# Kernel optimization log

Hardware: AMD Instinct MI355X
Metric: run time of the kernel (lower is better)

The kernel has to match this reference:

```python
import jax, jax.numpy as jnp
import numpy as np

SCORE_THRESHOLD = 0.05
IOU_THRESHOLD = 0.5
MAX_DETECTIONS = 300
NEG = -1e9  # sentinel for suppressed / below-threshold scores


def setup_inputs() -> dict:
    key = jax.random.key(0)
    k1, k2, k3, k4 = jax.random.split(key, 4)
    B, N, C = 8, 49104, 20
    # valid corner-format boxes [x1, y1, x2, y2] inside a 512x512 image
    ctr = jax.random.uniform(k1, (B, N, 2), minval=0.0, maxval=512.0)
    wh = jax.random.uniform(k2, (B, N, 2), minval=8.0, maxval=128.0)
    boxes = jnp.concatenate([ctr - wh / 2, ctr + wh / 2], axis=-1)
    boxes3D = jax.random.normal(k3, (B, N, 16), dtype=jnp.float32)
    classification = jax.random.uniform(k4, (B, N, C)) ** 2
    return {"boxes": boxes, "boxes3D": boxes3D, "classification": classification}


def _iou_one_vs_all(box, boxes, areas):
    # box [4], boxes [N,4], areas [N] -> iou [N]
    lt = jnp.maximum(box[:2], boxes[:, :2])
    rb = jnp.minimum(box[2:], boxes[:, 2:])
    wh = jnp.maximum(rb - lt, 0.0)
    inter = wh[:, 0] * wh[:, 1]
    area = (box[2] - box[0]) * (box[3] - box[1])
    return inter / (areas + area - inter + 1e-9)


def _nms_class(boxes, areas, scores):
    # greedy NMS for one class; fixed MAX_DETECTIONS iterations (jit-friendly)
    s0 = jnp.where(scores > SCORE_THRESHOLD, scores, NEG)
    n = scores.shape[0]
    arange_n = jnp.arange(n)

    def step(s, _):
        i = jnp.argmax(s)
        valid = s[i] > NEG / 2
        iou = _iou_one_vs_all(boxes[i], boxes, areas)
        sup = (iou > IOU_THRESHOLD) | (arange_n == i)
        s_new = jnp.where(valid & sup, NEG, s)
        return s_new, (i, jnp.where(valid, s[i], NEG))

    _, (idx, sel) = jax.lax.scan(step, s0, None, length=MAX_DETECTIONS)
    return idx, sel  # [MAX_DETECTIONS] each


def _filter_image(boxes, boxes3D, cls):
    # boxes [N,4], boxes3D [N,16], cls [N,C]
    areas = (boxes[:, 2] - boxes[:, 0]) * (boxes[:, 3] - boxes[:, 1])
    # per-class NMS, vectorized over classes
    idxs, scs = jax.vmap(lambda s: _nms_class(boxes, areas, s), in_axes=1)(cls)  # [C, MAX]
    C = cls.shape[1]
    labels = jnp.broadcast_to(jnp.arange(C)[:, None], idxs.shape)
    # global top-k across all class candidates (invalid ones carry NEG score)
    top_sc, top_i = jax.lax.top_k(scs.reshape(-1), MAX_DETECTIONS)
    sel_anchor = idxs.reshape(-1)[top_i]
    sel_lab = labels.reshape(-1)[top_i]
    ok = top_sc > NEG / 2
    out_boxes = jnp.where(ok[:, None], boxes[sel_anchor], -1.0)
    out_b3d = jnp.where(ok[:, None], boxes3D[sel_anchor], -1.0)
    out_sc = jnp.where(ok, top_sc, -1.0)
    out_lab = jnp.where(ok, sel_lab, -1).astype(jnp.int32)
    return out_boxes, out_b3d, out_sc, out_lab


def reference(boxes, boxes3D, classification):
    # map over batch, like backend.map_fn in the original
    return jax.vmap(_filter_image)(boxes, boxes3D, classification)
```

## Files before the change

### kernel.cpp

```cpp
#include <hip/hip_runtime.h>

#define NCLS    20
#define NB      8
#define MAXDET  300
#define NEGV    (-1e9f)
#define NEGH    (-5e8f)
#define BLKN    512
#define BLKC    1024
#define KTARGET 896
#define KMAX    1024
#define NBIN    256
#define NSLICE  64
#define SLSH    6
#define NSEG    8
#define SEGCAP  128
#define CSTR    16
#define T0F     0.98257f

#define T_MID   0x1.000001p-1

typedef unsigned long long u64;
typedef unsigned int u32;

__device__ __forceinline__ u64 packkey(float s, int j) {
    return ((u64)(__float_as_uint(s) ^ 0x80000000u) << 32) | (u32)(~(u32)j);
}
__device__ __forceinline__ u64 wredmax64(u64 k) {
#pragma unroll
    for (int off = 32; off > 0; off >>= 1) {
        u64 o = __shfl_xor(k, off);
        if (o > k) k = o;
    }
    return k;
}
__device__ __forceinline__ int binfull(float s) {
    int full = (int)(s * 262144.0f);
    return full > 262143 ? 262143 : full;
}
__device__ __forceinline__ int bin256(float s) { return binfull(s) >> 10; }

__global__ __launch_bounds__(256) void zero_kernel(u32* __restrict__ p, int nwords)
{
    int i = blockIdx.x * 256 + threadIdx.x;
    if (i < nwords) p[i] = 0;
}

__global__ __launch_bounds__(BLKN) void collect_kernel(
    const float* __restrict__ cls, u64* __restrict__ keys_g, u32* __restrict__ cnt_g, int n)
{
    const int b = blockIdx.x & 7;
    const int slice = blockIdx.x >> 3;
    const int seg = slice >> 3;
    const int tid = threadIdx.x;
    const int F4 = (n * NCLS) >> 2;
    const int s0 = (int)(((long)slice * F4) >> SLSH);
    const int s1 = (int)(((long)(slice + 1) * F4) >> SLSH);

    const float4* p4 = (const float4*)(cls + (long)b * n * NCLS);
    for (int q = s0 + tid; q < s1; q += BLKN) {
        float4 v = p4[q];
        int f = q << 2;
        float ss[4] = {v.x, v.y, v.z, v.w};
#pragma unroll
        for (int e = 0; e < 4; ++e) {
            float sc = ss[e];
            if (sc > T0F) {
                u32 fe = (u32)(f + e);
                u32 c = fe % NCLS;
                int row = (int)(fe / NCLS);
                const int pair = b * NCLS + (int)c;
                u32 slot = atomicAdd(&cnt_g[(pair * NSEG + seg) * CSTR], 1u);
                if (slot < SEGCAP)
                    keys_g[(long)pair * KMAX + (seg << 7) + slot] = packkey(sc, row);
            }
        }
    }
}

__device__ __forceinline__ u64 cmb(u64 e, u64 p, int i, int jj, int k2) {
    bool up = ((i & k2) == 0);
    bool low = ((i & jj) == 0);
    return (up == low) ? (e > p ? e : p) : (e < p ? e : p);
}
__device__ __forceinline__ void sort1024_1(u64& e, int tid, u64* bufA, u64* bufB) {
    int parity = 0;
    for (int k2 = 2; k2 <= 1024; k2 <<= 1) {
        for (int jj = k2 >> 1; jj > 0; jj >>= 1) {
            if (jj >= 64) {
                u64* buf = parity ? bufB : bufA; parity ^= 1;
                buf[tid] = e;
                __syncthreads();
                u64 p = buf[tid ^ jj];
                e = cmb(e, p, tid, jj, k2);
            } else {
                u64 p = __shfl_xor(e, jj);
                e = cmb(e, p, tid, jj, k2);
            }
        }
    }
    __syncthreads();
    bufA[tid] = e;
    __syncthreads();
}
__device__ __forceinline__ void sort512_1(u64& e, int tid, u64* bufA, u64* bufB) {
    int parity = 0;
    for (int k2 = 2; k2 <= 512; k2 <<= 1) {
        for (int jj = k2 >> 1; jj > 0; jj >>= 1) {
            if (jj >= 64) {
                u64* buf = parity ? bufB : bufA; parity ^= 1;
                if (tid < 512) buf[tid] = e;
                __syncthreads();
                if (tid < 512) { u64 p = buf[tid ^ jj]; e = cmb(e, p, tid, jj, k2); }
            } else {
                if (tid < 512) { u64 p = __shfl_xor(e, jj); e = cmb(e, p, tid, jj, k2); }
            }
        }
    }
    __syncthreads();
    if (tid < 512) bufA[tid] = e;
    __syncthreads();
}

template<bool PRE>
__global__ __launch_bounds__(BLKC, 1) void nms_final_kernel(
    const float4* __restrict__ boxes,
    const float*  __restrict__ cls,
    const u64* __restrict__ keys_g,
    const u32* __restrict__ cnt_g,
    float* __restrict__ sel_ws, int* __restrict__ idx_ws, int n)
{
    const int b = blockIdx.x & 7;
    const int c = blockIdx.x >> 3;
    const int pair = b * NCLS + c;
    const int tid = threadIdx.x;
    const int lane = tid & 63;
    const int wv = tid >> 6;

    const float4* bb = boxes + (long)b * n;
    const float* srow = cls + (long)b * n * NCLS + c;
    float* selp = sel_ws + pair * MAXDET;
    int*   idxp = idx_ws + pair * MAXDET;

    __shared__ u64    keysA[KMAX], keysB[KMAX];
    __shared__ float4 cbox[KMAX];
    __shared__ float4 aBox[MAXDET];
    __shared__ u32    hist256[NBIN];
    __shared__ u32    segc[NSEG];
    __shared__ u32    kb0[64], kb1[64], psupm[2];
    __shared__ u64    wl[16];
    __shared__ int    ctrl[8];
    __shared__ u64    ubk;

    if (PRE && tid < NSEG) segc[tid] = cnt_g[(pair * NSEG + tid) * CSTR];
    if (tid == 0) { ubk = ~0ull; ctrl[5] = 0; }
    if (tid < 64) { kb0[tid] = 0; kb1[tid] = 0; }
    if (tid < 2)  psupm[tid] = 0;
    bool first = true;
    __syncthreads();

    int pre_tot = 0; bool pre_ok = false;
    if (PRE) {
        bool over = false;
#pragma unroll
        for (int s = 0; s < NSEG; ++s) {
            int cv = (int)segc[s];
            pre_tot += cv;
            over = over || (cv > SEGCAP);
        }
        pre_ok = (!over) && (pre_tot > 0);
    }

    while (true) {
        const u64 UB = ubk;
        int trusted, cumTotal;

        if (PRE && first && pre_ok) {
            cumTotal = 0x7fffffff;
            trusted = pre_tot;
            keysA[tid] = 0;
            __syncthreads();
            {
                const int s = tid >> 7, r = tid & (SEGCAP - 1);
                if (r < (int)segc[s]) {
                    int start = 0;
#pragma unroll
                    for (int q = 0; q < NSEG; ++q) if (q < s) start += (int)segc[q];
                    keysA[start + r] = keys_g[(long)pair * KMAX + tid];
                }
            }
            __syncthreads();
            if (pre_tot <= 512) {
                u64 e = (tid < 512) ? keysA[tid] : 0;
                sort512_1(e, tid, keysA, keysB);
            } else {
                u64 e = keysA[tid];
                sort1024_1(e, tid, keysA, keysB);
            }
        } else {
            if (tid < NBIN) hist256[tid] = 0;
            keysA[tid] = 0;
            if (tid > 0 && tid < 5) ctrl[tid] = 0;
            if (tid == 0) ctrl[0] = -1;
            __syncthreads();
            for (int j = tid; j < n; j += BLKC) {
                float sc = srow[(long)j * NCLS];
                if (sc > 0.05f) { u64 ky = packkey(sc, j); if (ky < UB) atomicAdd(&hist256[bin256(sc)], 1u); }
            }
            __syncthreads();
            if (wv == 0) {
                u32 h0 = hist256[4 * lane], h1 = hist256[4 * lane + 1],
                    h2 = hist256[4 * lane + 2], h3 = hist256[4 * lane + 3];
                int acc = (int)(h0 + h1 + h2 + h3);
#pragma unroll
                for (int d = 1; d < 64; d <<= 1) { int o = __shfl_down(acc, d); if (lane + d < 64) acc += o; }
                int S0 = acc, S1 = S0 - (int)h0, S2 = S1 - (int)h1, S3 = S2 - (int)h2, S4 = S3 - (int)h3;
                if (lane == 0) { ctrl[0] = -1; ctrl[1] = 0; ctrl[2] = S0; }
                int bin = -1, ca = 0;
                if      (S0 >= KTARGET && S1 < KTARGET) { bin = 4 * lane;     ca = S1; }
                else if (S1 >= KTARGET && S2 < KTARGET) { bin = 4 * lane + 1; ca = S2; }
                else if (S2 >= KTARGET && S3 < KTARGET) { bin = 4 * lane + 2; ca = S3; }
                else if (S3 >= KTARGET && S4 < KTARGET) { bin = 4 * lane + 3; ca = S4; }
                if (bin >= 0) { ctrl[0] = bin; ctrl[1] = ca; }
            }
            __syncthreads();
            cumTotal = ctrl[2];
            if (cumTotal == 0) break;
            const int cumAbove = ctrl[1];
            const int B = ctrl[0];
            for (int j = tid; j < n; j += BLKC) {
                float sc = srow[(long)j * NCLS];
                if (sc > 0.05f) {
                    u64 ky = packkey(sc, j);
                    if (ky < UB) {
                        int bn = bin256(sc);
                        if (bn > B) { int sl = atomicAdd(&ctrl[4], 1); if (sl < KMAX) keysA[sl] = ky; }
                        else if (bn == B) {
                            int p = atomicAdd(&ctrl[3], 1);
                            int pos = KMAX - 1 - p;
                            if (pos >= cumAbove) keysA[pos] = ky;
                        }
                    }
                }
            }
            __syncthreads();
            const int cLo = ctrl[3], cHi = ctrl[4];
            const bool dropped = (cHi + cLo) > KMAX;
            trusted = dropped ? cHi : (cHi + cLo);
            if (trusted > 0) {
                u64 e = keysA[tid];
                __syncthreads();
                sort1024_1(e, tid, keysA, keysB);
            } else {
                u64 lb = 0;
                for (int j = tid; j < n; j += BLKC) {
                    float sc = srow[(long)j * NCLS];
                    if (sc > 0.05f) { u64 ky = packkey(sc, j); if (ky < UB && ky > lb) lb = ky; }
                }
                lb = wredmax64(lb);
                if (lane == 0) wl[wv] = lb;
                __syncthreads();
                if (tid == 0) { u64 bk = 0; for (int w = 0; w < 16; ++w) if (wl[w] > bk) bk = wl[w]; keysA[0] = bk; }
                trusted = 1;
                __syncthreads();
            }
        }

        {
            u64 ky = (tid < trusted) ? keysA[tid] : 0;
            float4 bx = make_float4(0.f, 0.f, 0.f, 0.f);
            if (tid < trusted) bx = bb[(int)(~(u32)ky)];
            cbox[tid] = bx;
        }
        __syncthreads();

        for (int base = 0; base < trusted; base += 64) {
            const int kcur = ctrl[5];
            if (kcur >= MAXDET) break;
            const int ci = base + lane;
            const bool have = ci < trusted;
            const float4 pb = cbox[have ? ci : 0];
            const float par = (pb.z - pb.x) * (pb.w - pb.y);

            bool sup = false;
            for (int a = wv; a < kcur; a += 16) {
                float4 ab = aBox[a];
                float am = (ab.z - ab.x) * (ab.w - ab.y);
                float ltx = fmaxf(ab.x, pb.x), lty = fmaxf(ab.y, pb.y);
                float rbx = fminf(ab.z, pb.z), rby = fminf(ab.w, pb.w);
                float wx = fmaxf(rbx - ltx, 0.0f), wy = fmaxf(rby - lty, 0.0f);
                float inter = wx * wy;
                float den = ((par + am) - inter) + 1e-9f;
                sup = sup || ((double)inter > T_MID * (double)den);
            }
            u64 bal = __ballot(sup && have);
            if (lane == 0 && bal) { atomicOr(&psupm[0], (u32)bal); atomicOr(&psupm[1], (u32)(bal >> 32)); }

#pragma unroll
            for (int r = 0; r < 4; ++r) {
                const int m = (r << 4) | wv;
                if (lane < m && (base + m) < trusted) {
                    float4 vb = cbox[base + m];
                    float va = (vb.z - vb.x) * (vb.w - vb.y);
                    float ltx = fmaxf(pb.x, vb.x), lty = fmaxf(pb.y, vb.y);
                    float rbx = fminf(pb.z, vb.z), rby = fminf(pb.w, vb.w);
                    float wx = fmaxf(rbx - ltx, 0.0f), wy = fmaxf(rby - lty, 0.0f);
                    float inter = wx * wy;
                    float den = ((va + par) - inter) + 1e-9f;
                    if ((double)inter > T_MID * (double)den) {
                        if (lane < 32) atomicOr(&kb0[m], 1u << lane);
                        else           atomicOr(&kb1[m], 1u << (lane - 32));
                    }
                }
            }
            __syncthreads();

            if (tid < 64) {
                const u64 kbm = ((u64)kb1[lane] << 32) | kb0[lane];
                const u64 ps  = ((u64)psupm[1] << 32) | psupm[0];
                const bool alive0 = have && !((ps >> lane) & 1);
                u64 accm = __ballot(alive0);
                for (int it = 0; it < 64; ++it) {
                    u64 nm = __ballot(alive0 && ((kbm & accm) == 0ull));
                    if (nm == accm) break;
                    accm = nm;
                }
                const bool a = (accm >> lane) & 1;
                const int rank = (int)__popcll(accm & ((1ull << lane) - 1ull));
                const int rem = MAXDET - kcur;
                if (a && rank < rem) {
                    const int slot = kcur + rank;
                    aBox[slot] = pb;
                    const u64 ky = keysA[ci];
                    selp[slot] = __uint_as_float((u32)(ky >> 32) ^ 0x80000000u);
                    idxp[slot] = (int)(~(u32)ky);
                }
                kb0[lane] = 0; kb1[lane] = 0;
                if (lane < 2) psupm[lane] = 0;
                if (lane == 0) {
                    const int cnt = (int)__popcll(accm);
                    ctrl[5] = kcur + (cnt < rem ? cnt : rem);
                }
            }
            __syncthreads();
        }

        if (tid == 0) ubk = keysA[trusted - 1];
        first = false;
        __syncthreads();
        if (ctrl[5] >= MAXDET || cumTotal - trusted <= 0) break;
    }

    const int kfin = ctrl[5];
    for (int f = kfin + tid; f < MAXDET; f += BLKC) { selp[f] = NEGV; idxp[f] = 0; }
}

#define OFF_B3D (NB * MAXDET * 4)
#define OFF_SC  (OFF_B3D + NB * MAXDET * 16)
#define OFF_LAB (OFF_SC + NB * MAXDET)

__global__ __launch_bounds__(1024, 1) void topk_kernel(
    const float4* __restrict__ boxes,
    const float*  __restrict__ b3d,
    const float*  __restrict__ sel_ws,
    const int*    __restrict__ idx_ws,
    float* __restrict__ out,
    int n)
{
    const int b = blockIdx.x;
    const int tid = threadIdx.x;
    const int lane = tid & 63;
    const int wv = tid >> 6;
    const int M = NCLS * MAXDET;

    __shared__ u64  kall[NCLS * MAXDET];
    __shared__ u32  h1[512];
    __shared__ u64  keysA[512], keysB[512];
    __shared__ int  wts[8], ews[8];
    __shared__ int  ctrl[8];
    __shared__ int  outA[MAXDET];

    const float* sp = sel_ws + b * M;
    for (int f = tid; f < M; f += 1024) {
        float v = sp[f];
        kall[f] = (v > 0.05f) ? packkey(v, f) : 0ull;
    }
    if (tid < 512) { h1[tid] = 0; keysA[tid] = 0; }
    if (tid > 0 && tid < 8) ctrl[tid] = 0;
    if (tid == 0) { ctrl[0] = -1; ctrl[5] = -1; }
    __syncthreads();

    for (int f = tid; f < M; f += 1024) {
        u64 k = kall[f];
        if (k) {
            float s = __uint_as_float((u32)(k >> 32) ^ 0x80000000u);
            atomicAdd(&h1[binfull(s) >> 9], 1u);
        }
    }
    __syncthreads();
    {
        const int h = (tid < 512) ? (int)h1[tid] : 0;
        int acc = h;
#pragma unroll
        for (int d = 1; d < 64; d <<= 1) { int o = __shfl_down(acc, d); if (lane + d < 64) acc += o; }
        if (lane == 0 && wv < 8) wts[wv] = acc;
        __syncthreads();
        if (tid < 8) { int e = 0; for (int w = tid + 1; w < 8; ++w) e += wts[w]; ews[tid] = e; }
        __syncthreads();
        if (tid < 512) {
            const int S = acc + ews[wv];
            if (S >= MAXDET && (S - h) < MAXDET) { ctrl[0] = tid; ctrl[1] = S - h; }
            if (tid == 0) ctrl[2] = S;
        }
    }
    __syncthreads();
    const int B1 = ctrl[0];
    const int cA1 = ctrl[1];

    if (tid < 512) h1[tid] = 0;
    __syncthreads();
    if (B1 >= 0) {
        for (int f = tid; f < M; f += 1024) {
            u64 k = kall[f];
            if (k) {
                float s = __uint_as_float((u32)(k >> 32) ^ 0x80000000u);
                int full = binfull(s);
                if ((full >> 9) == B1) atomicAdd(&h1[full & 511], 1u);
            }
        }
    }
    __syncthreads();
    const int KT2 = MAXDET - cA1;
    {
        const int h = (tid < 512) ? (int)h1[tid] : 0;
        int acc = h;
#pragma unroll
        for (int d = 1; d < 64; d <<= 1) { int o = __shfl_down(acc, d); if (lane + d < 64) acc += o; }
        if (lane == 0 && wv < 8) wts[wv] = acc;
        __syncthreads();
        if (tid < 8) { int e = 0; for (int w = tid + 1; w < 8; ++w) e += wts[w]; ews[tid] = e; }
        __syncthreads();
        if (tid < 512) {
            const int S = acc + ews[wv];
            if (B1 >= 0 && S >= KT2 && (S - h) < KT2) { ctrl[5] = tid; ctrl[6] = S - h; }
        }
    }
    __syncthreads();
    const int B2 = ctrl[5];
    const int cA2 = ctrl[6];

    for (int f = tid; f < M; f += 1024) {
        u64 k = kall[f];
        if (k) {
            float s = __uint_as_float((u32)(k >> 32) ^ 0x80000000u);
            int full = binfull(s);
            int bkt = full >> 9, sub = full & 511;
            bool hi = (B1 < 0) || (bkt > B1) || (bkt == B1 && sub > B2);
            bool lo = (B1 >= 0) && (bkt == B1) && (sub == B2);
            if (hi) { int slot = atomicAdd(&ctrl[3], 1); if (slot < 512) keysA[slot] = k; }
            else if (lo) { int p = atomicAdd(&ctrl[4], 1); int pos = 511 - p; if (pos >= cA1 + cA2) keysA[pos] = k; }
        }
    }
    __syncthreads();
    const bool dropped = (ctrl[3] + ctrl[4]) > 512;

    if (!dropped) {
        u64 e = (tid < 512) ? keysA[tid] : 0;
        int parity = 0;
        for (int k2 = 2; k2 <= 512; k2 <<= 1) {
            for (int jj = k2 >> 1; jj > 0; jj >>= 1) {
                if (jj >= 64) {
                    u64* buf = parity ? keysB : keysA; parity ^= 1;
                    if (tid < 512) buf[tid] = e;
                    __syncthreads();
                    if (tid < 512) { u64 p = buf[tid ^ jj]; e = cmb(e, p, tid, jj, k2); }
                } else {
                    if (tid < 512) { u64 p = __shfl_xor(e, jj); e = cmb(e, p, tid, jj, k2); }
                }
            }
        }
        __syncthreads();
        if (tid < 512) keysA[tid] = e;
        __syncthreads();
    } else {
        if (tid < 64) {
            int pos = 0;
            for (int k = 0; k < MAXDET; ++k) {
                u64 key = 0;
                if (lane < NCLS && pos < MAXDET) key = kall[lane * MAXDET + pos];
                u64 r = wredmax64(key);
                if (r != 0) {
                    u64 bal = __ballot(key == r);
                    int w = __ffsll((long long)bal) - 1;
                    if (lane == w) pos++;
                }
                if (lane == 0) keysA[k] = r;
            }
        }
        __syncthreads();
    }

    for (int k = tid; k < MAXDET; k += 1024) {
        const u64 kk = keysA[k];
        const bool ok = kk != 0;
        const int flat = (int)(~(u32)kk);
        const float sc = __uint_as_float((u32)(kk >> 32) ^ 0x80000000u);
        const int a = ok ? idx_ws[b * M + flat] : -1;
        const int cc = flat / MAXDET;
        float4 bx = make_float4(-1.f, -1.f, -1.f, -1.f);
        if (ok) bx = boxes[(long)b * n + a];
        out[(long)b * MAXDET * 4 + k * 4 + 0] = bx.x;
        out[(long)b * MAXDET * 4 + k * 4 + 1] = bx.y;
        out[(long)b * MAXDET * 4 + k * 4 + 2] = bx.z;
        out[(long)b * MAXDET * 4 + k * 4 + 3] = bx.w;
        out[OFF_SC  + (long)b * MAXDET + k] = ok ? sc : -1.0f;
        out[OFF_LAB + (long)b * MAXDET + k] = ok ? (float)cc : -1.0f;
        outA[k] = a;
    }
    __syncthreads();
    for (int q = tid; q < MAXDET * 16; q += 1024) {
        const int k = q >> 4;
        const int a = outA[k];
        out[OFF_B3D + (long)b * MAXDET * 16 + q] = (a >= 0) ? b3d[((long)b * n + a) * 16 + (q & 15)] : -1.0f;
    }
}

extern "C" void kernel_launch(void* const* d_in, const int* in_sizes, int n_in,
                              void* d_out, int out_size, void* d_ws, size_t ws_size,
                              hipStream_t stream)
{
    const float* boxes = (const float*)d_in[0];
    const float* b3d   = (const float*)d_in[1];
    const float* cls   = (const float*)d_in[2];
    float* out = (float*)d_out;

    const int n = in_sizes[0] / (NB * 4);
    const int NP = NB * NCLS;

    const size_t cntB   = (size_t)NP * NSEG * CSTR * sizeof(u32);
    const size_t keysB_ = (size_t)NP * KMAX * sizeof(u64);
    const size_t selB   = (size_t)NP * MAXDET * sizeof(float);

    char* p = (char*)d_ws;
    u32*  cnt_g  = (u32*)p;                p += cntB;
    u64*  keys_g = (u64*)p;                p += keysB_;
    float* sel_ws = (float*)p;             p += selB;
    int*   idx_ws = (int*)p;               p += selB;

    if (ws_size >= (size_t)(p - (char*)d_ws)) {
        const int zwords = (int)(cntB / sizeof(u32));
        hipLaunchKernelGGL(zero_kernel, dim3((zwords + 255) / 256), dim3(256), 0, stream,
                           cnt_g, zwords);
        hipLaunchKernelGGL(collect_kernel, dim3(NB * NSLICE), dim3(BLKN), 0, stream,
                           cls, keys_g, cnt_g, n);
        hipLaunchKernelGGL((nms_final_kernel<true>), dim3(NP), dim3(BLKC), 0, stream,
                           (const float4*)boxes, cls, keys_g, cnt_g, sel_ws, idx_ws, n);
        hipLaunchKernelGGL(topk_kernel, dim3(NB), dim3(1024), 0, stream,
                           (const float4*)boxes, b3d, sel_ws, idx_ws, out, n);
    } else {
        float* sel2 = (float*)d_ws;
        int*   idx2 = (int*)((char*)d_ws + selB);
        hipLaunchKernelGGL((nms_final_kernel<false>), dim3(NP), dim3(BLKC), 0, stream,
                           (const float4*)boxes, cls, nullptr, nullptr, sel2, idx2, n);
        hipLaunchKernelGGL(topk_kernel, dim3(NB), dim3(1024), 0, stream,
                           (const float4*)boxes, b3d, sel2, idx2, out, n);
    }
}
```

Before: 75.19 us.

## Fuse per-image top-k into NMS kernel via last-block-done counter

The last NMS block to finish for each image, detected with an atomic counter after a threadfence, now performs the histogram-based top-k selection and output gather. This removes the separate topk kernel launch and its global round trip on the main path. Top-k now runs on only 8 blocks at the tail of the NMS grid, and the fallback topk_kernel is reduced to a single-warp merge. The fused path needs extra shared memory and a reset of the done counter.

```diff
diff --git a/kernel.cpp b/kernel.cpp
--- a/kernel.cpp
+++ b/kernel.cpp
@@ -39,6 +39,10 @@
 }
 __device__ __forceinline__ int bin256(float s) { return binfull(s) >> 10; }
 
+#define OFF_B3D (NB * MAXDET * 4)
+#define OFF_SC  (OFF_B3D + NB * MAXDET * 16)
+#define OFF_LAB (OFF_SC + NB * MAXDET)
+
 __global__ __launch_bounds__(256) void zero_kernel(u32* __restrict__ p, int nwords)
 {
     int i = blockIdx.x * 256 + threadIdx.x;
@@ -125,9 +129,12 @@
 __global__ __launch_bounds__(BLKC, 1) void nms_final_kernel(
     const float4* __restrict__ boxes,
     const float*  __restrict__ cls,
+    const float*  __restrict__ b3d,
     const u64* __restrict__ keys_g,
     const u32* __restrict__ cnt_g,
-    float* __restrict__ sel_ws, int* __restrict__ idx_ws, int n)
+    u32* __restrict__ done_g,
+    float* __restrict__ sel_ws, int* __restrict__ idx_ws,
+    float* __restrict__ out, int n)
 {
     const int b = blockIdx.x & 7;
     const int c = blockIdx.x >> 3;
@@ -145,10 +152,13 @@
     __shared__ float4 cbox[KMAX];
     __shared__ float4 aBox[MAXDET];
     __shared__ u32    hist256[NBIN];
+    __shared__ u32    h512[512];
     __shared__ u32    segc[NSEG];
     __shared__ u32    kb0[64], kb1[64], psupm[2];
     __shared__ u64    wl[16];
+    __shared__ int    wts[8], ews[8];
     __shared__ int    ctrl[8];
+    __shared__ int    outA[MAXDET];
     __shared__ u64    ubk;
 
     if (PRE && tid < NSEG) segc[tid] = cnt_g[(pair * NSEG + tid) * CSTR];
@@ -352,11 +362,143 @@
 
     const int kfin = ctrl[5];
     for (int f = kfin + tid; f < MAXDET; f += BLKC) { selp[f] = NEGV; idxp[f] = 0; }
-}
-
-#define OFF_B3D (NB * MAXDET * 4)
-#define OFF_SC  (OFF_B3D + NB * MAXDET * 16)
-#define OFF_LAB (OFF_SC + NB * MAXDET)
+
+    if (done_g == nullptr) return;
+
+    __threadfence();
+    __syncthreads();
+    if (tid == 0) ctrl[6] = (int)atomicAdd(&done_g[b * CSTR], 1u);
+    __syncthreads();
+    if (ctrl[6] != NCLS - 1) return;
+    __threadfence();
+
+    const int M = NCLS * MAXDET;
+    const float* sp = sel_ws + b * M;
+    const int*   ip = idx_ws + b * M;
+
+    if (tid < 512) { h512[tid] = 0; keysA[tid] = 0; }
+    if (tid > 0 && tid < 8) ctrl[tid] = 0;
+    if (tid == 0) { ctrl[0] = -1; ctrl[5] = -1; }
+    __syncthreads();
+
+    for (int f = tid; f < M; f += BLKC) {
+        float v = sp[f];
+        if (v > 0.05f) atomicAdd(&h512[binfull(v) >> 9], 1u);
+    }
+    __syncthreads();
+    {
+        const int h = (tid < 512) ? (int)h512[tid] : 0;
+        int acc = h;
+#pragma unroll
+        for (int d = 1; d < 64; d <<= 1) { int o = __shfl_down(acc, d); if (lane + d < 64) acc += o; }
+        if (lane == 0 && wv < 8) wts[wv] = acc;
+        __syncthreads();
+        if (tid < 8) { int e = 0; for (int w = tid + 1; w < 8; ++w) e += wts[w]; ews[tid] = e; }
+        __syncthreads();
+        if (tid < 512) {
+            const int S = acc + ews[wv];
+            if (S >= MAXDET && (S - h) < MAXDET) { ctrl[0] = tid; ctrl[1] = S - h; }
+            if (tid == 0) ctrl[2] = S;
+        }
+    }
+    __syncthreads();
+    const int B1 = ctrl[0];
+    const int cA1 = ctrl[1];
+
+    if (tid < 512) h512[tid] = 0;
+    __syncthreads();
+    if (B1 >= 0) {
+        for (int f = tid; f < M; f += BLKC) {
+            float v = sp[f];
+            if (v > 0.05f) {
+                int full = binfull(v);
+                if ((full >> 9) == B1) atomicAdd(&h512[full & 511], 1u);
+            }
+        }
+    }
+    __syncthreads();
+    const int KT2 = MAXDET - cA1;
+    {
+        const int h = (tid < 512) ? (int)h512[tid] : 0;
+        int acc = h;
+#pragma unroll
+        for (int d = 1; d < 64; d <<= 1) { int o = __shfl_down(acc, d); if (lane + d < 64) acc += o; }
+        if (lane == 0 && wv < 8) wts[wv] = acc;
+        __syncthreads();
+        if (tid < 8) { int e = 0; for (int w = tid + 1; w < 8; ++w) e += wts[w]; ews[tid] = e; }
+        __syncthreads();
+        if (tid < 512) {
+            const int S = acc + ews[wv];
+            if (B1 >= 0 && S >= KT2 && (S - h) < KT2) { ctrl[5] = tid; ctrl[6] = S - h; }
+        }
+    }
+    __syncthreads();
+    const int B2 = ctrl[5];
+    const int cA2 = ctrl[6];
+
+    for (int f = tid; f < M; f += BLKC) {
+        float v = sp[f];
+        if (v > 0.05f) {
+            int full = binfull(v);
+            int bkt = full >> 9, sub = full & 511;
+            u64 k = packkey(v, f);
+            bool hi = (B1 < 0) || (bkt > B1) || (bkt == B1 && sub > B2);
+            bool lo = (B1 >= 0) && (bkt == B1) && (sub == B2);
+            if (hi) { int slot = atomicAdd(&ctrl[3], 1); if (slot < 512) keysA[slot] = k; }
+            else if (lo) { int p = atomicAdd(&ctrl[4], 1); int pos = 511 - p; if (pos >= cA1 + cA2) keysA[pos] = k; }
+        }
+    }
+    __syncthreads();
+    const bool tdrop = (ctrl[3] + ctrl[4]) > 512;
+
+    if (!tdrop) {
+        u64 e = (tid < 512) ? keysA[tid] : 0;
+        sort512_1(e, tid, keysA, keysB);
+    } else {
+        if (tid < 64) {
+            int pos = 0;
+            for (int k = 0; k < MAXDET; ++k) {
+                u64 key = 0;
+                if (lane < NCLS && pos < MAXDET) {
+                    float v = sp[lane * MAXDET + pos];
+                    if (v > 0.05f) key = packkey(v, lane * MAXDET + pos);
+                }
+                u64 r = wredmax64(key);
+                if (r != 0) {
+                    u64 bal = __ballot(key == r);
+                    int w = __ffsll((long long)bal) - 1;
+                    if (lane == w) pos++;
+                }
+                if (lane == 0) keysA[k] = r;
+            }
+        }
+        __syncthreads();
+    }
+
+    for (int k = tid; k < MAXDET; k += BLKC) {
+        const u64 kk = keysA[k];
+        const bool ok = kk != 0;
+        const int flat = (int)(~(u32)kk);
+        const float sc = __uint_as_float((u32)(kk >> 32) ^ 0x80000000u);
+        const int a = ok ? ip[flat] : -1;
+        const int cc = flat / MAXDET;
+        float4 bx = make_float4(-1.f, -1.f, -1.f, -1.f);
+        if (ok) bx = bb[a];
+        out[(long)b * MAXDET * 4 + k * 4 + 0] = bx.x;
+        out[(long)b * MAXDET * 4 + k * 4 + 1] = bx.y;
+        out[(long)b * MAXDET * 4 + k * 4 + 2] = bx.z;
+        out[(long)b * MAXDET * 4 + k * 4 + 3] = bx.w;
+        out[OFF_SC  + (long)b * MAXDET + k] = ok ? sc : -1.0f;
+        out[OFF_LAB + (long)b * MAXDET + k] = ok ? (float)cc : -1.0f;
+        outA[k] = a;
+    }
+    __syncthreads();
+    for (int q = tid; q < MAXDET * 16; q += BLKC) {
+        const int k = q >> 4;
+        const int a = outA[k];
+        out[OFF_B3D + (long)b * MAXDET * 16 + q] = (a >= 0) ? b3d[((long)b * n + a) * 16 + (q & 15)] : -1.0f;
+    }
+}
 
 __global__ __launch_bounds__(1024, 1) void topk_kernel(
     const float4* __restrict__ boxes,
@@ -369,135 +511,30 @@
     const int b = blockIdx.x;
     const int tid = threadIdx.x;
     const int lane = tid & 63;
-    const int wv = tid >> 6;
     const int M = NCLS * MAXDET;
 
-    __shared__ u64  kall[NCLS * MAXDET];
-    __shared__ u32  h1[512];
-    __shared__ u64  keysA[512], keysB[512];
-    __shared__ int  wts[8], ews[8];
-    __shared__ int  ctrl[8];
+    __shared__ u64  keysA[512];
     __shared__ int  outA[MAXDET];
 
-    const float* sp = sel_ws + b * M;
-    for (int f = tid; f < M; f += 1024) {
-        float v = sp[f];
-        kall[f] = (v > 0.05f) ? packkey(v, f) : 0ull;
-    }
-    if (tid < 512) { h1[tid] = 0; keysA[tid] = 0; }
-    if (tid > 0 && tid < 8) ctrl[tid] = 0;
-    if (tid == 0) { ctrl[0] = -1; ctrl[5] = -1; }
-    __syncthreads();
-
-    for (int f = tid; f < M; f += 1024) {
-        u64 k = kall[f];
-        if (k) {
-            float s = __uint_as_float((u32)(k >> 32) ^ 0x80000000u);
-            atomicAdd(&h1[binfull(s) >> 9], 1u);
-        }
-    }
-    __syncthreads();
-    {
-        const int h = (tid < 512) ? (int)h1[tid] : 0;
-        int acc = h;
-#pragma unroll
-        for (int d = 1; d < 64; d <<= 1) { int o = __shfl_down(acc, d); if (lane + d < 64) acc += o; }
-        if (lane == 0 && wv < 8) wts[wv] = acc;
-        __syncthreads();
-        if (tid < 8) { int e = 0; for (int w = tid + 1; w < 8; ++w) e += wts[w]; ews[tid] = e; }
-        __syncthreads();
-        if (tid < 512) {
-            const int S = acc + ews[wv];
-            if (S >= MAXDET && (S - h) < MAXDET) { ctrl[0] = tid; ctrl[1] = S - h; }
-            if (tid == 0) ctrl[2] = S;
-        }
-    }
-    __syncthreads();
-    const int B1 = ctrl[0];
-    const int cA1 = ctrl[1];
-
-    if (tid < 512) h1[tid] = 0;
-    __syncthreads();
-    if (B1 >= 0) {
-        for (int f = tid; f < M; f += 1024) {
-            u64 k = kall[f];
-            if (k) {
-                float s = __uint_as_float((u32)(k >> 32) ^ 0x80000000u);
-                int full = binfull(s);
-                if ((full >> 9) == B1) atomicAdd(&h1[full & 511], 1u);
-            }
-        }
-    }
-    __syncthreads();
-    const int KT2 = MAXDET - cA1;
-    {
-        const int h = (tid < 512) ? (int)h1[tid] : 0;
-        int acc = h;
-#pragma unroll
-        for (int d = 1; d < 64; d <<= 1) { int o = __shfl_down(acc, d); if (lane + d < 64) acc += o; }
-        if (lane == 0 && wv < 8) wts[wv] = acc;
-        __syncthreads();
-        if (tid < 8) { int e = 0; for (int w = tid + 1; w < 8; ++w) e += wts[w]; ews[tid] = e; }
-        __syncthreads();
-        if (tid < 512) {
-            const int S = acc + ews[wv];
-            if (B1 >= 0 && S >= KT2 && (S - h) < KT2) { ctrl[5] = tid; ctrl[6] = S - h; }
-        }
-    }
-    __syncthreads();
-    const int B2 = ctrl[5];
-    const int cA2 = ctrl[6];
-
-    for (int f = tid; f < M; f += 1024) {
-        u64 k = kall[f];
-        if (k) {
-            float s = __uint_as_float((u32)(k >> 32) ^ 0x80000000u);
-            int full = binfull(s);
-            int bkt = full >> 9, sub = full & 511;
-            bool hi = (B1 < 0) || (bkt > B1) || (bkt == B1 && sub > B2);
-            bool lo = (B1 >= 0) && (bkt == B1) && (sub == B2);
-            if (hi) { int slot = atomicAdd(&ctrl[3], 1); if (slot < 512) keysA[slot] = k; }
-            else if (lo) { int p = atomicAdd(&ctrl[4], 1); int pos = 511 - p; if (pos >= cA1 + cA2) keysA[pos] = k; }
-        }
-    }
-    __syncthreads();
-    const bool dropped = (ctrl[3] + ctrl[4]) > 512;
-
-    if (!dropped) {
-        u64 e = (tid < 512) ? keysA[tid] : 0;
-        int parity = 0;
-        for (int k2 = 2; k2 <= 512; k2 <<= 1) {
-            for (int jj = k2 >> 1; jj > 0; jj >>= 1) {
-                if (jj >= 64) {
-                    u64* buf = parity ? keysB : keysA; parity ^= 1;
-                    if (tid < 512) buf[tid] = e;
-                    __syncthreads();
-                    if (tid < 512) { u64 p = buf[tid ^ jj]; e = cmb(e, p, tid, jj, k2); }
-                } else {
-                    if (tid < 512) { u64 p = __shfl_xor(e, jj); e = cmb(e, p, tid, jj, k2); }
-                }
-            }
-        }
-        __syncthreads();
-        if (tid < 512) keysA[tid] = e;
-        __syncthreads();
-    } else {
-        if (tid < 64) {
-            int pos = 0;
-            for (int k = 0; k < MAXDET; ++k) {
-                u64 key = 0;
-                if (lane < NCLS && pos < MAXDET) key = kall[lane * MAXDET + pos];
-                u64 r = wredmax64(key);
-                if (r != 0) {
-                    u64 bal = __ballot(key == r);
-                    int w = __ffsll((long long)bal) - 1;
-                    if (lane == w) pos++;
-                }
-                if (lane == 0) keysA[k] = r;
-            }
-        }
-        __syncthreads();
-    }
+    if (tid < 64) {
+        int pos = 0;
+        const float* sp = sel_ws + b * M;
+        for (int k = 0; k < MAXDET; ++k) {
+            u64 key = 0;
+            if (lane < NCLS && pos < MAXDET) {
+                float v = sp[lane * MAXDET + pos];
+                if (v > 0.05f) key = packkey(v, lane * MAXDET + pos);
+            }
+            u64 r = wredmax64(key);
+            if (r != 0) {
+                u64 bal = __ballot(key == r);
+                int w = __ffsll((long long)bal) - 1;
+                if (lane == w) pos++;
+            }
+            if (lane == 0) keysA[k] = r;
+        }
+    }
+    __syncthreads();
 
     for (int k = tid; k < MAXDET; k += 1024) {
         const u64 kk = keysA[k];
@@ -537,30 +574,32 @@
     const int NP = NB * NCLS;
 
     const size_t cntB   = (size_t)NP * NSEG * CSTR * sizeof(u32);
+    const size_t doneB  = (size_t)NB * CSTR * sizeof(u32);
     const size_t keysB_ = (size_t)NP * KMAX * sizeof(u64);
     const size_t selB   = (size_t)NP * MAXDET * sizeof(float);
 
     char* p = (char*)d_ws;
     u32*  cnt_g  = (u32*)p;                p += cntB;
+    u32*  done_g = (u32*)p;                p += doneB;
     u64*  keys_g = (u64*)p;                p += keysB_;
     float* sel_ws = (float*)p;             p += selB;
     int*   idx_ws = (int*)p;               p += selB;
 
     if (ws_size >= (size_t)(p - (char*)d_ws)) {
-        const int zwords = (int)(cntB / sizeof(u32));
+        const int zwords = (int)((cntB + doneB) / sizeof(u32));
         hipLaunchKernelGGL(zero_kernel, dim3((zwords + 255) / 256), dim3(256), 0, stream,
                            cnt_g, zwords);
         hipLaunchKernelGGL(collect_kernel, dim3(NB * NSLICE), dim3(BLKN), 0, stream,
                            cls, keys_g, cnt_g, n);
         hipLaunchKernelGGL((nms_final_kernel<true>), dim3(NP), dim3(BLKC), 0, stream,
-                           (const float4*)boxes, cls, keys_g, cnt_g, sel_ws, idx_ws, n);
-        hipLaunchKernelGGL(topk_kernel, dim3(NB), dim3(1024), 0, stream,
-                           (const float4*)boxes, b3d, sel_ws, idx_ws, out, n);
+                           (const float4*)boxes, cls, b3d, keys_g, cnt_g, done_g,
+                           sel_ws, idx_ws, out, n);
     } else {
         float* sel2 = (float*)d_ws;
         int*   idx2 = (int*)((char*)d_ws + selB);
         hipLaunchKernelGGL((nms_final_kernel<false>), dim3(NP), dim3(BLKC), 0, stream,
-                           (const float4*)boxes, cls, nullptr, nullptr, sel2, idx2, n);
+                           (const float4*)boxes, cls, b3d, nullptr, nullptr, nullptr,
+                           sel2, idx2, out, n);
         hipLaunchKernelGGL(topk_kernel, dim3(NB), dim3(1024), 0, stream,
                            (const float4*)boxes, b3d, sel2, idx2, out, n);
     }
```

After: 111.6 us. 1.48x slower.
